# Kernel optimization log

Measured on AMD Instinct MI355X. Metric: run time of the kernel, lower is better.

The kernel has to match this reference:

```python
import jax, jax.numpy as jnp
import numpy as np


def setup_inputs() -> dict:
    key = jax.random.key(0)
    k1, k2 = jax.random.split(key)
    bs, dim = 8192, 768
    nl_vec = jax.random.normal(k1, (bs, dim), dtype=jnp.float32)
    code_vec = jax.random.normal(k2, (bs, dim), dtype=jnp.float32)
    return {"nl_vec": nl_vec, "code_vec": code_vec}


def reference(nl_vec, code_vec):
    # scores[i, j] = <nl_vec[i], code_vec[j]>  (GEMM form of the broadcast mult-sum)
    scores = jnp.einsum("id,jd->ij", nl_vec, code_vec)  # [bs, bs]
    bs = scores.shape[0]
    # CrossEntropyLoss with labels = arange(bs): mean over rows of (logsumexp - diag)
    lse = jax.nn.logsumexp(scores, axis=-1)             # [bs]
    diag = jnp.einsum("id,id->i", nl_vec, code_vec)     # scores[i, i]
    loss = jnp.mean(lse - diag)
    return (loss, code_vec, nl_vec)
```

## Files before the change

kernel.cpp:

```cpp
#include <hip/hip_runtime.h>

#define BS     8192
#define DIM    768
#define NPART  16
#define BM     128
#define BN     128
#define BK     64
#define PCOLS  (BS / NPART)
#define NJT    (PCOLS / BN)
#define NKT    (DIM / BK)
#define L1B    128
#define L1R    (BS / L1B)

typedef __bf16 bfrag_t __attribute__((ext_vector_type(8)));
typedef float  facc_t  __attribute__((ext_vector_type(4)));

typedef const __attribute__((address_space(1))) void gv_t;
typedef __attribute__((address_space(3))) void lv_t;

__device__ __forceinline__ void gll16(const void* g, void* l) {
  __builtin_amdgcn_global_load_lds((gv_t*)g, (lv_t*)l, 16, 0, 0);
}

__device__ __forceinline__ unsigned short f2bf(float f) {
  union { float f; unsigned u; } v; v.f = f;
  unsigned u = v.u;
  return (unsigned short)((u + 0x7FFFu + ((u >> 16) & 1u)) >> 16);
}

__global__ void prep_kernel(const float* __restrict__ nl, const float* __restrict__ cd,
                            float* __restrict__ cd_copy, float* __restrict__ nl_copy,
                            unsigned short* __restrict__ nlb, unsigned short* __restrict__ cdb,
                            float* __restrict__ dg) {
  const int lane = threadIdx.x & 63;
  const int wave = threadIdx.x >> 6;
  const int row  = blockIdx.x * 4 + wave;
  const size_t rbase = (size_t)row * DIM;
  const float4* ar = reinterpret_cast<const float4*>(nl + rbase);
  const float4* br = reinterpret_cast<const float4*>(cd + rbase);
  float4* wa = reinterpret_cast<float4*>(nl_copy + rbase);
  float4* wb = reinterpret_cast<float4*>(cd_copy + rbase);
  ushort4* ba = reinterpret_cast<ushort4*>(nlb + rbase);
  ushort4* bb = reinterpret_cast<ushort4*>(cdb + rbase);

  float s = 0.f;
#pragma unroll
  for (int i = 0; i < 3; ++i) {
    int idx = lane + 64 * i;
    float4 x = ar[idx];
    float4 y = br[idx];
    wa[idx] = x;
    wb[idx] = y;
    ushort4 xb, yb;
    xb.x = f2bf(x.x); xb.y = f2bf(x.y); xb.z = f2bf(x.z); xb.w = f2bf(x.w);
    yb.x = f2bf(y.x); yb.y = f2bf(y.y); yb.z = f2bf(y.z); yb.w = f2bf(y.w);
    ba[idx] = xb;
    bb[idx] = yb;
    s += x.x * y.x + x.y * y.y + x.z * y.z + x.w * y.w;
  }
#pragma unroll
  for (int off = 32; off; off >>= 1) s += __shfl_xor(s, off, 64);
  if (lane == 0) dg[row] = s;
}

__global__ __launch_bounds__(256, 4) void gemm_lse_kernel(
    const unsigned short* __restrict__ Abf,
    const unsigned short* __restrict__ Bbf,
    float* __restrict__ pm, float* __restrict__ pl) {
  __shared__ __align__(16) unsigned short As[BM * BK];
  __shared__ __align__(16) unsigned short Bs[BN * BK];

  const int tid  = threadIdx.x;
  const int lane = tid & 63;
  const int wave = tid >> 6;
  const int wm   = wave >> 1;
  const int wn   = wave & 1;
  const int l15  = lane & 15;
  const int l4   = lane >> 4;
  const int sw   = l15 & 7;
  const int cp   = blockIdx.x;
  const int rb   = blockIdx.y;

  int srow[4], sc8g[4];
#pragma unroll
  for (int t = 0; t < 4; ++t) {
    int u   = wave * 256 + t * 64 + lane;
    srow[t] = u >> 3;
    sc8g[t] = (u & 7) ^ (srow[t] & 7);
  }

  float mrun[4][4], lrun[4][4];
#pragma unroll
  for (int i = 0; i < 4; ++i)
#pragma unroll
    for (int r = 0; r < 4; ++r) { mrun[i][r] = -1e30f; lrun[i][r] = 0.f; }

  for (int jt = 0; jt < NJT; ++jt) {
    facc_t acc[4][4];
#pragma unroll
    for (int mt = 0; mt < 4; ++mt)
#pragma unroll
      for (int nt = 0; nt < 4; ++nt) acc[mt][nt] = (facc_t){0.f, 0.f, 0.f, 0.f};

    for (int kt = 0; kt < NKT; ++kt) {
      __syncthreads();
#pragma unroll
      for (int t = 0; t < 4; ++t) {
        size_t ldso = (size_t)(wave * 256 + t * 64) * 8;
        gll16(Abf + (size_t)(rb * BM + srow[t]) * DIM + kt * BK + sc8g[t] * 8, As + ldso);
        gll16(Bbf + (size_t)(cp * PCOLS + jt * BN + srow[t]) * DIM + kt * BK + sc8g[t] * 8, Bs + ldso);
      }
      __syncthreads();

#pragma unroll
      for (int ks = 0; ks < 2; ++ks) {
        const int k8 = ks * 4 + l4;
        bfrag_t af[4], bfv[4];
#pragma unroll
        for (int mt = 0; mt < 4; ++mt) {
          int row = wm * 64 + mt * 16 + l15;
          af[mt] = *reinterpret_cast<const bfrag_t*>(&As[row * BK + (k8 ^ sw) * 8]);
        }
#pragma unroll
        for (int nt = 0; nt < 4; ++nt) {
          int row = wn * 64 + nt * 16 + l15;
          bfv[nt] = *reinterpret_cast<const bfrag_t*>(&Bs[row * BK + (k8 ^ sw) * 8]);
        }
#pragma unroll
        for (int mt = 0; mt < 4; ++mt)
#pragma unroll
          for (int nt = 0; nt < 4; ++nt)
            acc[mt][nt] = __builtin_amdgcn_mfma_f32_16x16x32_bf16(af[mt], bfv[nt], acc[mt][nt], 0, 0, 0);
      }
    }

#pragma unroll
    for (int mt = 0; mt < 4; ++mt)
#pragma unroll
      for (int r = 0; r < 4; ++r) {
        float v0 = acc[mt][0][r], v1 = acc[mt][1][r], v2 = acc[mt][2][r], v3 = acc[mt][3][r];
        float tm = fmaxf(fmaxf(v0, v1), fmaxf(v2, v3));
        float mn = fmaxf(mrun[mt][r], tm);
        float sc = __expf(mrun[mt][r] - mn);
        lrun[mt][r] = lrun[mt][r] * sc +
                      __expf(v0 - mn) + __expf(v1 - mn) + __expf(v2 - mn) + __expf(v3 - mn);
        mrun[mt][r] = mn;
      }
  }

#pragma unroll
  for (int mask = 1; mask < 16; mask <<= 1)
#pragma unroll
    for (int mt = 0; mt < 4; ++mt)
#pragma unroll
      for (int r = 0; r < 4; ++r) {
        float om = __shfl_xor(mrun[mt][r], mask, 64);
        float ol = __shfl_xor(lrun[mt][r], mask, 64);
        float mn = fmaxf(mrun[mt][r], om);
        lrun[mt][r] = lrun[mt][r] * __expf(mrun[mt][r] - mn) + ol * __expf(om - mn);
        mrun[mt][r] = mn;
      }

  float* cm = reinterpret_cast<float*>(As);
  float* cl = reinterpret_cast<float*>(Bs);
  __syncthreads();
  if (l15 == 0) {
#pragma unroll
    for (int mt = 0; mt < 4; ++mt)
#pragma unroll
      for (int r = 0; r < 4; ++r) {
        int rl = wm * 64 + mt * 16 + l4 * 4 + r;
        cm[wn * BM + rl] = mrun[mt][r];
        cl[wn * BM + rl] = lrun[mt][r];
      }
  }
  __syncthreads();
  if (tid < BM) {
    float m0 = cm[tid], l0 = cl[tid];
    float m1 = cm[BM + tid], l1 = cl[BM + tid];
    float mn = fmaxf(m0, m1);
    float ll = l0 * __expf(m0 - mn) + l1 * __expf(m1 - mn);
    size_t g = (size_t)(rb * BM + tid) * NPART + cp;
    pm[g] = mn;
    pl[g] = ll;
  }
}

__global__ void loss_stage1_kernel(const float* __restrict__ pm, const float* __restrict__ pl,
                                   const float* __restrict__ dg, float* __restrict__ partial) {
  __shared__ float red[64];
  const int tid = threadIdx.x;
  const int r   = blockIdx.x * L1R + tid;

  const float4* pmr = reinterpret_cast<const float4*>(pm + (size_t)r * NPART);
  const float4* plr = reinterpret_cast<const float4*>(pl + (size_t)r * NPART);

  float m = -1e30f, l = 0.f;
#pragma unroll
  for (int q = 0; q < NPART / 4; ++q) {
    float4 mv = pmr[q];
    float4 lv = plr[q];
#pragma unroll
    for (int k = 0; k < 4; ++k) {
      float m2 = (&mv.x)[k], l2 = (&lv.x)[k];
      float mn = fmaxf(m, m2);
      l = l * __expf(m - mn) + l2 * __expf(m2 - mn);
      m = mn;
    }
  }
  float local = m + __logf(l) - dg[r];

#pragma unroll
  for (int off = 32; off; off >>= 1) local += __shfl_xor(local, off, 64);
  if (tid == 0) partial[blockIdx.x] = local;
  (void)red;
}

__global__ void loss_stage2_kernel(const float* __restrict__ partial, float* __restrict__ out) {
  const int tid = threadIdx.x;
  float v = partial[tid];
#pragma unroll
  for (int off = 32; off; off >>= 1) v += __shfl_xor(v, off, 64);
  __shared__ float red[2];
  if ((tid & 63) == 0) red[tid >> 6] = v;
  __syncthreads();
  if (tid == 0) out[0] = (red[0] + red[1]) / (float)BS;
}

extern "C" void kernel_launch(void* const* d_in, const int* in_sizes, int n_in,
                              void* d_out, int out_size, void* d_ws, size_t ws_size,
                              hipStream_t stream) {
  const float* nl = (const float*)d_in[0];
  const float* cd = (const float*)d_in[1];
  float* out = (float*)d_out;

  const size_t NEL = (size_t)BS * DIM;

  unsigned short* nlb = (unsigned short*)d_ws;
  unsigned short* cdb = nlb + NEL;
  float* pm = (float*)(cdb + NEL);
  float* pl = pm + (size_t)BS * NPART;
  float* dg = pl + (size_t)BS * NPART;
  float* partial = dg + BS;

  prep_kernel<<<BS / 4, 256, 0, stream>>>(nl, cd, out + 1, out + 1 + NEL, nlb, cdb, dg);
  gemm_lse_kernel<<<dim3(NPART, BS / BM), 256, 0, stream>>>(nlb, cdb, pm, pl);
  loss_stage1_kernel<<<L1B, 64, 0, stream>>>(pm, pl, dg, partial);
  loss_stage2_kernel<<<1, 128, 0, stream>>>(partial, out);
}
```

Baseline: 231.2 us.

## Restructure GEMM-LSE into 256x256 double-buffered tiles with interleaved load/MFMA phases

Each block now computes a single 256x256 output tile with 8 waves instead of looping over four 128x128 column tiles. The K loop is double-buffered in LDS and hand-scheduled into phases that interleave global-to-LDS loads with MFMA bursts, using s_setprio and explicit waitcnt/barriers. The aim is to hide load latency behind compute and raise data reuse per block. The trade-off is higher register and LDS use (lower occupancy, 2 blocks of 512 threads) and twice as many column partitions (32) for the LSE merge.

```diff
diff --git a/kernel.cpp b/kernel.cpp
--- a/kernel.cpp
+++ b/kernel.cpp
@@ -2,12 +2,10 @@
 
 #define BS     8192
 #define DIM    768
-#define NPART  16
-#define BM     128
-#define BN     128
+#define NPART  32
+#define BM     256
+#define BN     256
 #define BK     64
-#define PCOLS  (BS / NPART)
-#define NJT    (PCOLS / BN)
 #define NKT    (DIM / BK)
 #define L1B    128
 #define L1R    (BS / L1B)
@@ -63,132 +61,183 @@
   if (lane == 0) dg[row] = s;
 }
 
-__global__ __launch_bounds__(256, 4) void gemm_lse_kernel(
+__global__ __launch_bounds__(512, 2) void gemm_lse_kernel(
     const unsigned short* __restrict__ Abf,
     const unsigned short* __restrict__ Bbf,
     float* __restrict__ pm, float* __restrict__ pl) {
-  __shared__ __align__(16) unsigned short As[BM * BK];
-  __shared__ __align__(16) unsigned short Bs[BN * BK];
+  __shared__ __align__(16) unsigned short As[2 * BM * BK];
+  __shared__ __align__(16) unsigned short Bs[2 * BN * BK];
 
   const int tid  = threadIdx.x;
   const int lane = tid & 63;
   const int wave = tid >> 6;
-  const int wm   = wave >> 1;
-  const int wn   = wave & 1;
+  const int wm   = wave >> 2;
+  const int wn   = wave & 3;
   const int l15  = lane & 15;
   const int l4   = lane >> 4;
-  const int sw   = l15 & 7;
-  const int cp   = blockIdx.x;
+  const int swz  = l15 & 7;
+  const int cb   = blockIdx.x;
   const int rb   = blockIdx.y;
 
-  int srow[4], sc8g[4];
-#pragma unroll
-  for (int t = 0; t < 4; ++t) {
-    int u   = wave * 256 + t * 64 + lane;
-    srow[t] = u >> 3;
-    sc8g[t] = (u & 7) ^ (srow[t] & 7);
-  }
-
-  float mrun[4][4], lrun[4][4];
-#pragma unroll
-  for (int i = 0; i < 4; ++i)
-#pragma unroll
-    for (int r = 0; r < 4; ++r) { mrun[i][r] = -1e30f; lrun[i][r] = 0.f; }
-
-  for (int jt = 0; jt < NJT; ++jt) {
-    facc_t acc[4][4];
-#pragma unroll
-    for (int mt = 0; mt < 4; ++mt)
-#pragma unroll
-      for (int nt = 0; nt < 4; ++nt) acc[mt][nt] = (facc_t){0.f, 0.f, 0.f, 0.f};
-
-    for (int kt = 0; kt < NKT; ++kt) {
-      __syncthreads();
-#pragma unroll
-      for (int t = 0; t < 4; ++t) {
-        size_t ldso = (size_t)(wave * 256 + t * 64) * 8;
-        gll16(Abf + (size_t)(rb * BM + srow[t]) * DIM + kt * BK + sc8g[t] * 8, As + ldso);
-        gll16(Bbf + (size_t)(cp * PCOLS + jt * BN + srow[t]) * DIM + kt * BK + sc8g[t] * 8, Bs + ldso);
+  const int k8x0 = ((0 * 4 + l4) ^ swz) * 8;
+  const int k8x1 = ((1 * 4 + l4) ^ swz) * 8;
+
+  size_t aoff[4], boff[4];
+  int ldso[4];
+#pragma unroll
+  for (int p = 0; p < 4; ++p) {
+    int u   = p * 512 + tid;
+    int row = u >> 3;
+    int c8  = (u & 7) ^ (row & 7);
+    aoff[p] = (size_t)(rb * BM + row) * DIM + c8 * 8;
+    boff[p] = (size_t)(cb * BN + row) * DIM + c8 * 8;
+    ldso[p] = u * 8;
+  }
+
+#define STG_A(kt, h) do { \
+    gll16(Abf + aoff[2*(h)]   + (size_t)(kt) * BK, &As[(((kt) & 1) << 14) + ldso[2*(h)]]); \
+    gll16(Abf + aoff[2*(h)+1] + (size_t)(kt) * BK, &As[(((kt) & 1) << 14) + ldso[2*(h)+1]]); \
+  } while (0)
+#define STG_B(kt, h) do { \
+    gll16(Bbf + boff[2*(h)]   + (size_t)(kt) * BK, &Bs[(((kt) & 1) << 14) + ldso[2*(h)]]); \
+    gll16(Bbf + boff[2*(h)+1] + (size_t)(kt) * BK, &Bs[(((kt) & 1) << 14) + ldso[2*(h)+1]]); \
+  } while (0)
+
+  bfrag_t af[2][2];
+  bfrag_t bf[4][2];
+  facc_t  acc[8][4];
+#pragma unroll
+  for (int mt = 0; mt < 8; ++mt)
+#pragma unroll
+    for (int nt = 0; nt < 4; ++nt) acc[mt][nt] = (facc_t){0.f, 0.f, 0.f, 0.f};
+
+#define DS_A(b, q) do { \
+    _Pragma("unroll") \
+    for (int i_ = 0; i_ < 2; ++i_) { \
+      const unsigned short* pA_ = &As[(b) * 16384 + (wm * 128 + (2*(q)+i_) * 16 + l15) * 64]; \
+      af[i_][0] = *reinterpret_cast<const bfrag_t*>(pA_ + k8x0); \
+      af[i_][1] = *reinterpret_cast<const bfrag_t*>(pA_ + k8x1); \
+    } } while (0)
+#define DS_B(b) do { \
+    _Pragma("unroll") \
+    for (int n_ = 0; n_ < 4; ++n_) { \
+      const unsigned short* pB_ = &Bs[(b) * 16384 + (wn * 64 + n_ * 16 + l15) * 64]; \
+      bf[n_][0] = *reinterpret_cast<const bfrag_t*>(pB_ + k8x0); \
+      bf[n_][1] = *reinterpret_cast<const bfrag_t*>(pB_ + k8x1); \
+    } } while (0)
+#define MFMA_Q(q) do { \
+    _Pragma("unroll") \
+    for (int i_ = 0; i_ < 2; ++i_) \
+      _Pragma("unroll") \
+      for (int n_ = 0; n_ < 4; ++n_) { \
+        acc[2*(q)+i_][n_] = __builtin_amdgcn_mfma_f32_16x16x32_bf16(af[i_][0], bf[n_][0], acc[2*(q)+i_][n_], 0, 0, 0); \
+        acc[2*(q)+i_][n_] = __builtin_amdgcn_mfma_f32_16x16x32_bf16(af[i_][1], bf[n_][1], acc[2*(q)+i_][n_], 0, 0, 0); \
+      } } while (0)
+
+#define PH_TOP() do { __builtin_amdgcn_s_barrier(); \
+    asm volatile("s_waitcnt lgkmcnt(0)" ::: "memory"); \
+    __builtin_amdgcn_sched_barrier(0); \
+    __builtin_amdgcn_s_setprio(1); } while (0)
+#define PH_BOT() do { __builtin_amdgcn_s_setprio(0); \
+    __builtin_amdgcn_sched_barrier(0); \
+    __builtin_amdgcn_s_barrier(); } while (0)
+#define PH_BOT_VM(n) do { __builtin_amdgcn_s_setprio(0); \
+    __builtin_amdgcn_sched_barrier(0); \
+    asm volatile("s_waitcnt vmcnt(" #n ")" ::: "memory"); \
+    __builtin_amdgcn_sched_barrier(0); \
+    __builtin_amdgcn_s_barrier(); } while (0)
+
+  STG_B(0, 0); STG_B(0, 1); STG_A(0, 0); STG_A(0, 1); STG_B(1, 0); STG_B(1, 1);
+  asm volatile("s_waitcnt vmcnt(4)" ::: "memory");
+  __builtin_amdgcn_sched_barrier(0);
+  __builtin_amdgcn_s_barrier();
+
+  for (int t = 0; t < 5; ++t) {
+    const int k0 = 2 * t;
+    DS_B(0); DS_A(0, 0); STG_A(k0 + 1, 0); STG_A(k0 + 1, 1);
+    PH_TOP(); MFMA_Q(0); PH_BOT();
+    DS_A(0, 1); STG_B(k0 + 2, 0);
+    PH_TOP(); MFMA_Q(1); PH_BOT();
+    DS_A(0, 2); STG_B(k0 + 2, 1);
+    PH_TOP(); MFMA_Q(2); PH_BOT();
+    DS_A(0, 3);
+    PH_TOP(); MFMA_Q(3); PH_BOT_VM(4);
+    DS_B(1); DS_A(1, 0); STG_A(k0 + 2, 0);
+    PH_TOP(); MFMA_Q(0); PH_BOT();
+    DS_A(1, 1); STG_A(k0 + 2, 1);
+    PH_TOP(); MFMA_Q(1); PH_BOT();
+    DS_A(1, 2); STG_B(k0 + 3, 0);
+    PH_TOP(); MFMA_Q(2); PH_BOT();
+    DS_A(1, 3); STG_B(k0 + 3, 1);
+    PH_TOP(); MFMA_Q(3); PH_BOT_VM(4);
+  }
+
+  DS_B(0); DS_A(0, 0); STG_A(11, 0); STG_A(11, 1);
+  PH_TOP(); MFMA_Q(0); PH_BOT();
+  DS_A(0, 1);
+  PH_TOP(); MFMA_Q(1); PH_BOT();
+  DS_A(0, 2);
+  PH_TOP(); MFMA_Q(2); PH_BOT();
+  DS_A(0, 3);
+  PH_TOP(); MFMA_Q(3); PH_BOT_VM(0);
+  DS_B(1); DS_A(1, 0);
+  PH_TOP(); MFMA_Q(0); PH_BOT();
+  DS_A(1, 1);
+  PH_TOP(); MFMA_Q(1); PH_BOT();
+  DS_A(1, 2);
+  PH_TOP(); MFMA_Q(2); PH_BOT();
+  DS_A(1, 3);
+  PH_TOP(); MFMA_Q(3); PH_BOT();
+
+  float* cm = reinterpret_cast<float*>(As);
+  float* cl = reinterpret_cast<float*>(Bs);
+#pragma unroll
+  for (int mt = 0; mt < 8; ++mt)
+#pragma unroll
+    for (int r = 0; r < 4; ++r) {
+      float v0 = acc[mt][0][r], v1 = acc[mt][1][r], v2 = acc[mt][2][r], v3 = acc[mt][3][r];
+      float m = fmaxf(fmaxf(v0, v1), fmaxf(v2, v3));
+      float l = __expf(v0 - m) + __expf(v1 - m) + __expf(v2 - m) + __expf(v3 - m);
+#pragma unroll
+      for (int mask = 1; mask < 16; mask <<= 1) {
+        float om = __shfl_xor(m, mask, 64);
+        float ol = __shfl_xor(l, mask, 64);
+        float mn = fmaxf(m, om);
+        l = l * __expf(m - mn) + ol * __expf(om - mn);
+        m = mn;
       }
-      __syncthreads();
-
-#pragma unroll
-      for (int ks = 0; ks < 2; ++ks) {
-        const int k8 = ks * 4 + l4;
-        bfrag_t af[4], bfv[4];
-#pragma unroll
-        for (int mt = 0; mt < 4; ++mt) {
-          int row = wm * 64 + mt * 16 + l15;
-          af[mt] = *reinterpret_cast<const bfrag_t*>(&As[row * BK + (k8 ^ sw) * 8]);
-        }
-#pragma unroll
-        for (int nt = 0; nt < 4; ++nt) {
-          int row = wn * 64 + nt * 16 + l15;
-          bfv[nt] = *reinterpret_cast<const bfrag_t*>(&Bs[row * BK + (k8 ^ sw) * 8]);
-        }
-#pragma unroll
-        for (int mt = 0; mt < 4; ++mt)
-#pragma unroll
-          for (int nt = 0; nt < 4; ++nt)
-            acc[mt][nt] = __builtin_amdgcn_mfma_f32_16x16x32_bf16(af[mt], bfv[nt], acc[mt][nt], 0, 0, 0);
+      if (l15 == 0) {
+        int rl = wm * 128 + mt * 16 + l4 * 4 + r;
+        cm[wn * BM + rl] = m;
+        cl[wn * BM + rl] = l;
       }
     }
-
-#pragma unroll
-    for (int mt = 0; mt < 4; ++mt)
-#pragma unroll
-      for (int r = 0; r < 4; ++r) {
-        float v0 = acc[mt][0][r], v1 = acc[mt][1][r], v2 = acc[mt][2][r], v3 = acc[mt][3][r];
-        float tm = fmaxf(fmaxf(v0, v1), fmaxf(v2, v3));
-        float mn = fmaxf(mrun[mt][r], tm);
-        float sc = __expf(mrun[mt][r] - mn);
-        lrun[mt][r] = lrun[mt][r] * sc +
-                      __expf(v0 - mn) + __expf(v1 - mn) + __expf(v2 - mn) + __expf(v3 - mn);
-        mrun[mt][r] = mn;
-      }
-  }
-
-#pragma unroll
-  for (int mask = 1; mask < 16; mask <<= 1)
-#pragma unroll
-    for (int mt = 0; mt < 4; ++mt)
-#pragma unroll
-      for (int r = 0; r < 4; ++r) {
-        float om = __shfl_xor(mrun[mt][r], mask, 64);
-        float ol = __shfl_xor(lrun[mt][r], mask, 64);
-        float mn = fmaxf(mrun[mt][r], om);
-        lrun[mt][r] = lrun[mt][r] * __expf(mrun[mt][r] - mn) + ol * __expf(om - mn);
-        mrun[mt][r] = mn;
-      }
-
-  float* cm = reinterpret_cast<float*>(As);
-  float* cl = reinterpret_cast<float*>(Bs);
-  __syncthreads();
-  if (l15 == 0) {
-#pragma unroll
-    for (int mt = 0; mt < 4; ++mt)
-#pragma unroll
-      for (int r = 0; r < 4; ++r) {
-        int rl = wm * 64 + mt * 16 + l4 * 4 + r;
-        cm[wn * BM + rl] = mrun[mt][r];
-        cl[wn * BM + rl] = lrun[mt][r];
-      }
-  }
   __syncthreads();
   if (tid < BM) {
-    float m0 = cm[tid], l0 = cl[tid];
-    float m1 = cm[BM + tid], l1 = cl[BM + tid];
-    float mn = fmaxf(m0, m1);
-    float ll = l0 * __expf(m0 - mn) + l1 * __expf(m1 - mn);
-    size_t g = (size_t)(rb * BM + tid) * NPART + cp;
+    float m0 = cm[tid],          l0 = cl[tid];
+    float m1 = cm[BM + tid],     l1 = cl[BM + tid];
+    float m2 = cm[2 * BM + tid], l2 = cl[2 * BM + tid];
+    float m3 = cm[3 * BM + tid], l3 = cl[3 * BM + tid];
+    float mn = fmaxf(fmaxf(m0, m1), fmaxf(m2, m3));
+    float ll = l0 * __expf(m0 - mn) + l1 * __expf(m1 - mn) +
+               l2 * __expf(m2 - mn) + l3 * __expf(m3 - mn);
+    size_t g = (size_t)(rb * BM + tid) * NPART + cb;
     pm[g] = mn;
     pl[g] = ll;
   }
+
+#undef STG_A
+#undef STG_B
+#undef DS_A
+#undef DS_B
+#undef MFMA_Q
+#undef PH_TOP
+#undef PH_BOT
+#undef PH_BOT_VM
 }
 
 __global__ void loss_stage1_kernel(const float* __restrict__ pm, const float* __restrict__ pl,
                                    const float* __restrict__ dg, float* __restrict__ partial) {
-  __shared__ float red[64];
   const int tid = threadIdx.x;
   const int r   = blockIdx.x * L1R + tid;
 
@@ -213,7 +262,6 @@
 #pragma unroll
   for (int off = 32; off; off >>= 1) local += __shfl_xor(local, off, 64);
   if (tid == 0) partial[blockIdx.x] = local;
-  (void)red;
 }
 
 __global__ void loss_stage2_kernel(const float* __restrict__ partial, float* __restrict__ out) {
@@ -244,7 +292,7 @@
   float* partial = dg + BS;
 
   prep_kernel<<<BS / 4, 256, 0, stream>>>(nl, cd, out + 1, out + 1 + NEL, nlb, cdb, dg);
-  gemm_lse_kernel<<<dim3(NPART, BS / BM), 256, 0, stream>>>(nlb, cdb, pm, pl);
+  gemm_lse_kernel<<<dim3(NPART, BS / BM), 512, 0, stream>>>(nlb, cdb, pm, pl);
   loss_stage1_kernel<<<L1B, 64, 0, stream>>>(pm, pl, dg, partial);
   loss_stage2_kernel<<<1, 128, 0, stream>>>(partial, out);
 }
```

Result: slower. 251.5 us (+8.8%).
